# Optimization experiments

Measured on AMD Instinct MI355X. Metric: run time of the kernel, lower is better.

The kernel has to match this reference:

```python
import jax, jax.numpy as jnp
import numpy as np

P = 8192  # num_particles
C = 8192  # num EEG channels (must equal P for the original broadcast to be valid)


def setup_inputs() -> dict:
    key = jax.random.key(0)
    k1, k2, k3, k4, k5 = jax.random.split(key, 5)
    inputs = jax.random.normal(k1, (1, C, P), dtype=jnp.float32)
    state_vector = jax.random.normal(k2, (P, 3), dtype=jnp.float32)
    # near-identity transition for numerical sanity
    transition_matrix = jnp.eye(3, dtype=jnp.float32) + 0.01 * jax.random.normal(k3, (3, 3), dtype=jnp.float32)
    # symmetric positive-definite process noise covariance (Cholesky must succeed)
    a = jax.random.normal(k4, (3, 3), dtype=jnp.float32)
    process_noise_cov = 0.01 * (a @ a.T) + 0.1 * jnp.eye(3, dtype=jnp.float32)
    forward_matrix = jax.random.normal(k5, (C, 3), dtype=jnp.float32)
    return {
        "inputs": inputs,
        "state_vector": state_vector,
        "transition_matrix": transition_matrix,
        "process_noise_cov": process_noise_cov,
        "forward_matrix": forward_matrix,
    }


def reference(inputs, state_vector, transition_matrix, process_noise_cov, forward_matrix):
    k_noise, k_cat = jax.random.split(jax.random.key(42))
    # --- state transition: x_new = x @ T^T + eps,  eps ~ N(0, Q) via z @ chol(Q) ---
    updated = state_vector @ transition_matrix.T                      # (P, 3)
    L = jnp.linalg.cholesky(process_noise_cov)                        # (3, 3) lower
    z = jax.random.normal(k_noise, (P, 3), dtype=state_vector.dtype)
    state = updated + z @ L                                           # (P, 3)
    # --- EEG measurement model: H @ x^T -> (C, P) ---
    predicted = forward_matrix @ state.T                              # (C, P)
    # --- particle weights: squared-residual sum (broadcast (1,C,P) - (P,C), C==P) ---
    w = jnp.sum(jnp.square(inputs - predicted.T), axis=-1)[0]         # (P,)
    # --- categorical resampling on log-weights (unnormalized logits) ---
    idx = jax.random.categorical(k_cat, jnp.log(w), shape=(P,))       # (P,) int
    resampled = state[idx]                                            # (P, 3) gather
    return jnp.mean(resampled, axis=0)                                # (3,)
```

## Files before the change

kernel.cpp:

```cpp
#include <hip/hip_runtime.h>
#include <stdint.h>

#define NP 8192
#define NC 8192

__host__ __device__ inline uint32_t rotl32(uint32_t x, int r) {
  return __builtin_rotateleft32(x, (unsigned)r);
}

__host__ __device__ inline void threefry2x32(uint32_t k0, uint32_t k1,
                                             uint32_t x0, uint32_t x1,
                                             uint32_t& o0, uint32_t& o1) {
  uint32_t ks2 = k0 ^ k1 ^ 0x1BD11BDAu;
  x0 += k0; x1 += k1;
#define TF_R(r) { x0 += x1; x1 = rotl32(x1, (r)); x1 ^= x0; }
  TF_R(13) TF_R(15) TF_R(26) TF_R(6)   x0 += k1;  x1 += ks2 + 1u;
  TF_R(17) TF_R(29) TF_R(16) TF_R(24)  x0 += ks2; x1 += k0 + 2u;
  TF_R(13) TF_R(15) TF_R(26) TF_R(6)   x0 += k0;  x1 += k1 + 3u;
  TF_R(17) TF_R(29) TF_R(16) TF_R(24)  x0 += k1;  x1 += ks2 + 4u;
  TF_R(13) TF_R(15) TF_R(26) TF_R(6)   x0 += ks2; x1 += k0 + 5u;
#undef TF_R
  o0 = x0; o1 = x1;
}

__device__ inline uint32_t tf_bits(uint32_t k0, uint32_t k1, uint32_t i) {
  uint32_t o0, o1;
  threefry2x32(k0, k1, 0u, i, o0, o1);
  return o0 ^ o1;
}

__device__ inline float u01(uint32_t bits) {
  return __uint_as_float((bits >> 9) | 0x3f800000u) - 1.0f;
}

__device__ inline float erfinvf_(float x) {
  float w = -log1pf(-x * x);
  float p;
  if (w < 5.0f) {
    w -= 2.5f;
    p = 2.81022636e-08f;
    p = fmaf(p, w, 3.43273939e-07f);
    p = fmaf(p, w, -3.5233877e-06f);
    p = fmaf(p, w, -4.39150654e-06f);
    p = fmaf(p, w, 0.00021858087f);
    p = fmaf(p, w, -0.00125372503f);
    p = fmaf(p, w, -0.00417768164f);
    p = fmaf(p, w, 0.246640727f);
    p = fmaf(p, w, 1.50140941f);
  } else {
    w = sqrtf(w) - 3.0f;
    p = -0.000200214257f;
    p = fmaf(p, w, 0.000100950558f);
    p = fmaf(p, w, 0.00134934322f);
    p = fmaf(p, w, -0.00367342844f);
    p = fmaf(p, w, 0.00573950773f);
    p = fmaf(p, w, -0.0076224613f);
    p = fmaf(p, w, 0.00943887047f);
    p = fmaf(p, w, 1.00167406f);
    p = fmaf(p, w, 2.83297682f);
  }
  return p * x;
}

__global__ void __launch_bounds__(256) k_prep(uint32_t k0, uint32_t k1,
                                              const float* __restrict__ sv,
                                              const float* __restrict__ T,
                                              const float* __restrict__ Q,
                                              const float* __restrict__ H,
                                              float* __restrict__ st,
                                              float* __restrict__ ht) {
  int b = blockIdx.x;
  if (b < 32) {
    int i = b * 256 + threadIdx.x;
    const float lo = -0.99999994f;
    float zz[3];
#pragma unroll
    for (int k = 0; k < 3; k++) {
      uint32_t bits = tf_bits(k0, k1, 3u * (uint32_t)i + (uint32_t)k);
      float v = fmaxf(lo, u01(bits) * 2.0f + lo);
      zz[k] = 1.41421356f * erfinvf_(v);
    }
    float L00 = sqrtf(Q[0]);
    float L10 = Q[3] / L00, L20 = Q[6] / L00;
    float L11 = sqrtf(Q[4] - L10 * L10);
    float L21 = (Q[7] - L20 * L10) / L11;
    float L22 = sqrtf(Q[8] - L20 * L20 - L21 * L21);
    float s0 = sv[i * 3], s1 = sv[i * 3 + 1], s2 = sv[i * 3 + 2];
    float u0 = s0 * T[0] + s1 * T[1] + s2 * T[2];
    float u1 = s0 * T[3] + s1 * T[4] + s2 * T[5];
    float u2 = s0 * T[6] + s1 * T[7] + s2 * T[8];
    st[i * 3]     = u0 + (zz[0] * L00 + zz[1] * L10 + zz[2] * L20);
    st[i * 3 + 1] = u1 + (zz[1] * L11 + zz[2] * L21);
    st[i * 3 + 2] = u2 + (zz[2] * L22);
  } else {
    int t = (b - 32) * 256 + threadIdx.x;
    int k = t >> 13, j = t & (NP - 1);
    ht[t] = H[j * 3 + k];
  }
}

__global__ void __launch_bounds__(256) k_weights(const float* __restrict__ in,
                                                 const float* __restrict__ ht,
                                                 const float* __restrict__ st,
                                                 float* __restrict__ winv) {
  int wave = threadIdx.x >> 6;
  int lane = threadIdx.x & 63;
  int row = blockIdx.x * 4 + wave;
  float s0 = st[row * 3], s1 = st[row * 3 + 1], s2 = st[row * 3 + 2];
  const float4* inrow = (const float4*)(in + (size_t)row * NC);
  const float4* h0 = (const float4*)ht;
  const float4* h1 = (const float4*)(ht + NC);
  const float4* h2 = (const float4*)(ht + 2 * NC);
  float acc = 0.0f;
#pragma unroll 4
  for (int it = lane; it < NC / 4; it += 64) {
    float4 x = inrow[it];
    float4 a = h0[it];
    float4 b = h1[it];
    float4 c = h2[it];
    float d0 = x.x - (a.x * s0 + b.x * s1 + c.x * s2);
    float d1 = x.y - (a.y * s0 + b.y * s1 + c.y * s2);
    float d2 = x.z - (a.z * s0 + b.z * s1 + c.z * s2);
    float d3 = x.w - (a.w * s0 + b.w * s1 + c.w * s2);
    acc += d0 * d0 + d1 * d1 + d2 * d2 + d3 * d3;
  }
#pragma unroll
  for (int off = 32; off > 0; off >>= 1) acc += __shfl_down(acc, off, 64);
  if (lane == 0) winv[row] = 1.0f / acc;
}

__global__ void __launch_bounds__(256) k_resample(uint32_t k0, uint32_t k1,
                                                  const float* __restrict__ winv,
                                                  int* __restrict__ idx) {
  uint32_t s = blockIdx.x;
  uint32_t base = s * (uint32_t)NP;
  const float TINY = 1.17549435e-38f;
  float best = 3.4e38f;
  int bi = 0;
#pragma unroll 4
  for (uint32_t i = threadIdx.x; i < NP; i += 256) {
    uint32_t bits = tf_bits(k0, k1, base + i);
    float v = fmaxf(u01(bits), TINY);
    float r = -__logf(v) * winv[i];
    if (r < best) { best = r; bi = (int)i; }
  }
  __shared__ float rv[256];
  __shared__ int ri[256];
  rv[threadIdx.x] = best;
  ri[threadIdx.x] = bi;
  __syncthreads();
  for (int stp = 128; stp > 0; stp >>= 1) {
    if (threadIdx.x < stp) {
      float va = rv[threadIdx.x], vb = rv[threadIdx.x + stp];
      int ia = ri[threadIdx.x], ib = ri[threadIdx.x + stp];
      if (vb < va || (vb == va && ib < ia)) { rv[threadIdx.x] = vb; ri[threadIdx.x] = ib; }
    }
    __syncthreads();
  }
  if (threadIdx.x == 0) idx[s] = ri[0];
}

__global__ void __launch_bounds__(1024) k_mean(const float* __restrict__ st,
                                               const int* __restrict__ idx,
                                               float* __restrict__ out) {
  double a0 = 0, a1 = 0, a2 = 0;
  for (int s = threadIdx.x; s < NP; s += 1024) {
    int j = idx[s];
    a0 += st[j * 3];
    a1 += st[j * 3 + 1];
    a2 += st[j * 3 + 2];
  }
  __shared__ double r0[1024], r1[1024], r2[1024];
  r0[threadIdx.x] = a0; r1[threadIdx.x] = a1; r2[threadIdx.x] = a2;
  __syncthreads();
  for (int s = 512; s > 0; s >>= 1) {
    if (threadIdx.x < s) {
      r0[threadIdx.x] += r0[threadIdx.x + s];
      r1[threadIdx.x] += r1[threadIdx.x + s];
      r2[threadIdx.x] += r2[threadIdx.x + s];
    }
    __syncthreads();
  }
  if (threadIdx.x == 0) {
    out[0] = (float)(r0[0] / NP);
    out[1] = (float)(r1[0] / NP);
    out[2] = (float)(r2[0] / NP);
  }
}

extern "C" void kernel_launch(void* const* d_in, const int* in_sizes, int n_in,
                              void* d_out, int out_size, void* d_ws, size_t ws_size,
                              hipStream_t stream) {
  const float* in = (const float*)d_in[0];
  const float* sv = (const float*)d_in[1];
  const float* T  = (const float*)d_in[2];
  const float* Q  = (const float*)d_in[3];
  const float* H  = (const float*)d_in[4];
  float* out = (float*)d_out;

  float* st   = (float*)d_ws;
  float* ht   = st + 24576;
  float* winv = ht + 24576;
  int*   idx  = (int*)(winv + NP);

  uint32_t nk0, nk1, ck0, ck1;
  threefry2x32(0u, 42u, 0u, 0u, nk0, nk1);
  threefry2x32(0u, 42u, 0u, 1u, ck0, ck1);

  hipLaunchKernelGGL(k_prep, dim3(128), dim3(256), 0, stream, nk0, nk1, sv, T, Q, H, st, ht);
  hipLaunchKernelGGL(k_weights, dim3(NP / 4), dim3(256), 0, stream, in, ht, st, winv);
  hipLaunchKernelGGL(k_resample, dim3(NP), dim3(256), 0, stream, ck0, ck1, winv, idx);
  hipLaunchKernelGGL(k_mean, dim3(1), dim3(1024), 0, stream, st, idx, out);
}
```

Measured before the change: 562.8 us.

## Overlap exponential-noise generation with weight reduction via a workspace buffer

Splits resampling into two phases. A fused kernel interleaves the memory-bound weight-computation blocks with compute-bound Threefry/log blocks that write all P×P exponential variates into a 256 MB workspace. A separate race kernel then multiplies them by the inverse weights and takes the argmin. The aim is to hide the RNG compute under the input-streaming bandwidth. The cost is writing and re-reading a 256 MB buffer, and the fast path only runs when the workspace is large enough.

```diff
diff --git a/kernel.cpp b/kernel.cpp
--- a/kernel.cpp
+++ b/kernel.cpp
@@ -31,6 +31,13 @@
 
 __device__ inline float u01(uint32_t bits) {
   return __uint_as_float((bits >> 9) | 0x3f800000u) - 1.0f;
+}
+
+__device__ inline float egen(uint32_t k0, uint32_t k1, uint32_t ctr) {
+  const float TINY = 1.17549435e-38f;
+  uint32_t bits = tf_bits(k0, k1, ctr);
+  float v = fmaxf(u01(bits), TINY);
+  return -__logf(v);
 }
 
 __device__ inline float erfinvf_(float x) {
@@ -99,6 +106,89 @@
   }
 }
 
+__global__ void __launch_bounds__(256) k_fused(uint32_t k0, uint32_t k1,
+                                               const float* __restrict__ in,
+                                               const float* __restrict__ ht,
+                                               const float* __restrict__ st,
+                                               float* __restrict__ winv,
+                                               float* __restrict__ E) {
+  int b = blockIdx.x;
+  if (b % 5 == 0) {
+    int w = b / 5;
+    int wave = threadIdx.x >> 6;
+    int lane = threadIdx.x & 63;
+    int row = w * 4 + wave;
+    float s0 = st[row * 3], s1 = st[row * 3 + 1], s2 = st[row * 3 + 2];
+    const float4* inrow = (const float4*)(in + (size_t)row * NC);
+    const float4* h0 = (const float4*)ht;
+    const float4* h1 = (const float4*)(ht + NC);
+    const float4* h2 = (const float4*)(ht + 2 * NC);
+    float acc = 0.0f;
+#pragma unroll 4
+    for (int it = lane; it < NC / 4; it += 64) {
+      float4 x = inrow[it];
+      float4 a = h0[it];
+      float4 bb = h1[it];
+      float4 c = h2[it];
+      float d0 = x.x - (a.x * s0 + bb.x * s1 + c.x * s2);
+      float d1 = x.y - (a.y * s0 + bb.y * s1 + c.y * s2);
+      float d2 = x.z - (a.z * s0 + bb.z * s1 + c.z * s2);
+      float d3 = x.w - (a.w * s0 + bb.w * s1 + c.w * s2);
+      acc += d0 * d0 + d1 * d1 + d2 * d2 + d3 * d3;
+    }
+#pragma unroll
+    for (int off = 32; off > 0; off >>= 1) acc += __shfl_down(acc, off, 64);
+    if (lane == 0) winv[row] = 1.0f / acc;
+  } else {
+    int s = b - b / 5 - 1;
+    uint32_t base = (uint32_t)s * (uint32_t)NP;
+    float4* erow = (float4*)(E + (size_t)s * NP);
+#pragma unroll 2
+    for (int p = 0; p < 8; ++p) {
+      uint32_t i0 = (uint32_t)(p * 1024 + 4 * threadIdx.x);
+      float4 e;
+      e.x = egen(k0, k1, base + i0);
+      e.y = egen(k0, k1, base + i0 + 1u);
+      e.z = egen(k0, k1, base + i0 + 2u);
+      e.w = egen(k0, k1, base + i0 + 3u);
+      erow[i0 >> 2] = e;
+    }
+  }
+}
+
+__global__ void __launch_bounds__(256) k_race(const float* __restrict__ E,
+                                              const float* __restrict__ winv,
+                                              int* __restrict__ idx) {
+  int wave = threadIdx.x >> 6;
+  int lane = threadIdx.x & 63;
+  int s = blockIdx.x * 4 + wave;
+  const float4* erow = (const float4*)(E + (size_t)s * NP);
+  const float4* wv = (const float4*)winv;
+  float best = 3.4e38f;
+  int bi = 0;
+#pragma unroll 4
+  for (int it = lane; it < NP / 4; it += 64) {
+    float4 e = erow[it];
+    float4 w = wv[it];
+    int i = it * 4;
+    float r0 = e.x * w.x;
+    float r1 = e.y * w.y;
+    float r2 = e.z * w.z;
+    float r3 = e.w * w.w;
+    if (r0 < best) { best = r0; bi = i; }
+    if (r1 < best) { best = r1; bi = i + 1; }
+    if (r2 < best) { best = r2; bi = i + 2; }
+    if (r3 < best) { best = r3; bi = i + 3; }
+  }
+#pragma unroll
+  for (int off = 32; off > 0; off >>= 1) {
+    float ob = __shfl_down(best, off, 64);
+    int oi = __shfl_down(bi, off, 64);
+    if (ob < best || (ob == best && oi < bi)) { best = ob; bi = oi; }
+  }
+  if (lane == 0) idx[s] = bi;
+}
+
 __global__ void __launch_bounds__(256) k_weights(const float* __restrict__ in,
                                                  const float* __restrict__ ht,
                                                  const float* __restrict__ st,
@@ -198,17 +288,34 @@
   const float* H  = (const float*)d_in[4];
   float* out = (float*)d_out;
 
-  float* st   = (float*)d_ws;
-  float* ht   = st + 24576;
-  float* winv = ht + 24576;
-  int*   idx  = (int*)(winv + NP);
-
   uint32_t nk0, nk1, ck0, ck1;
   threefry2x32(0u, 42u, 0u, 0u, nk0, nk1);
   threefry2x32(0u, 42u, 0u, 1u, ck0, ck1);
 
-  hipLaunchKernelGGL(k_prep, dim3(128), dim3(256), 0, stream, nk0, nk1, sv, T, Q, H, st, ht);
-  hipLaunchKernelGGL(k_weights, dim3(NP / 4), dim3(256), 0, stream, in, ht, st, winv);
-  hipLaunchKernelGGL(k_resample, dim3(NP), dim3(256), 0, stream, ck0, ck1, winv, idx);
-  hipLaunchKernelGGL(k_mean, dim3(1), dim3(1024), 0, stream, st, idx, out);
-}
+  const size_t eFloats = (size_t)NP * (size_t)NP;
+  const size_t tailBytes = (24576 + 24576 + NP + NP) * 4;
+  const bool fused = ws_size >= eFloats * 4 + tailBytes;
+
+  if (fused) {
+    float* E    = (float*)d_ws;
+    float* st   = E + eFloats;
+    float* ht   = st + 24576;
+    float* winv = ht + 24576;
+    int*   idx  = (int*)(winv + NP);
+
+    hipLaunchKernelGGL(k_prep, dim3(128), dim3(256), 0, stream, nk0, nk1, sv, T, Q, H, st, ht);
+    hipLaunchKernelGGL(k_fused, dim3(10240), dim3(256), 0, stream, ck0, ck1, in, ht, st, winv, E);
+    hipLaunchKernelGGL(k_race, dim3(NP / 4), dim3(256), 0, stream, E, winv, idx);
+    hipLaunchKernelGGL(k_mean, dim3(1), dim3(1024), 0, stream, st, idx, out);
+  } else {
+    float* st   = (float*)d_ws;
+    float* ht   = st + 24576;
+    float* winv = ht + 24576;
+    int*   idx  = (int*)(winv + NP);
+
+    hipLaunchKernelGGL(k_prep, dim3(128), dim3(256), 0, stream, nk0, nk1, sv, T, Q, H, st, ht);
+    hipLaunchKernelGGL(k_weights, dim3(NP / 4), dim3(256), 0, stream, in, ht, st, winv);
+    hipLaunchKernelGGL(k_resample, dim3(NP), dim3(256), 0, stream, ck0, ck1, winv, idx);
+    hipLaunchKernelGGL(k_mean, dim3(1), dim3(1024), 0, stream, st, idx, out);
+  }
+}
```

Result: faster. 527.9 us (-6.2%).
